# Kernel tuning notes

Hardware: AMD Instinct MI355X
Metric: run time of the kernel (lower is better)

The kernel has to match this reference:

```python
import jax, jax.numpy as jnp
import numpy as np

B, C, D, H, W = 4, 32, 64, 64, 64
RATIO = 2
K = 7  # spatial conv kernel


def setup_inputs() -> dict:
    key = jax.random.key(0)
    ks = jax.random.split(key, 7)
    x = jax.random.normal(ks[0], (B, C, D, H, W), dtype=jnp.float32)
    # ChannelAttention params (torch Linear: y = x @ W.T + b)
    fc1_w = jax.random.normal(ks[1], (2 * C * RATIO, 2 * C), dtype=jnp.float32) * 0.05
    fc1_b = jax.random.normal(ks[2], (2 * C * RATIO,), dtype=jnp.float32) * 0.05
    fc2_w = jax.random.normal(ks[3], (C, 2 * C * RATIO), dtype=jnp.float32) * 0.05
    fc2_b = jax.random.normal(ks[4], (C,), dtype=jnp.float32) * 0.05
    # SpatialAttention convs (no bias): conv1 2->4 k=7 pad 3, conv2 4->1 k=1
    conv1_w = jax.random.normal(ks[5], (2 * RATIO, 2, K, K, K), dtype=jnp.float32) * 0.05
    conv2_w = jax.random.normal(ks[6], (1, 2 * RATIO, 1, 1, 1), dtype=jnp.float32) * 0.05
    return {"x": x, "fc1_w": fc1_w, "fc1_b": fc1_b, "fc2_w": fc2_w,
            "fc2_b": fc2_b, "conv1_w": conv1_w, "conv2_w": conv2_w}


def _conv3d(x, w, padding):
    return jax.lax.conv_general_dilated(
        x, w, window_strides=(1, 1, 1), padding=padding,
        dimension_numbers=("NCDHW", "OIDHW", "NCDHW"))


def reference(x, fc1_w, fc1_b, fc2_w, fc2_b, conv1_w, conv2_w):
    # --- ChannelAttention: ca [B, C] ---
    x_avg = jnp.mean(x, axis=(2, 3, 4))  # [B, C]
    x_max = jnp.max(x, axis=(2, 3, 4))   # [B, C]
    h = jnp.concatenate([x_avg, x_max], axis=1)  # [B, 2C]
    h = jax.nn.relu(h @ fc1_w.T + fc1_b)
    ca = jax.nn.sigmoid(h @ fc2_w.T + fc2_b)     # [B, C]

    # --- SpatialAttention: sa [B, 1, D, H, W] ---
    avg_out = jnp.mean(x, axis=1, keepdims=True)
    max_out = jnp.max(x, axis=1, keepdims=True)
    s = jnp.concatenate([avg_out, max_out], axis=1)  # [B, 2, D, H, W]
    s = jax.nn.relu(_conv3d(s, conv1_w, "SAME"))     # k=7, pad=3 == SAME
    sa = jax.nn.sigmoid(_conv3d(s, conv2_w, "VALID"))  # [B, 1, D, H, W]

    # fused broadcast replacing the per-(i,j) python loop:
    # attention[b, c] = sa[b, 0] * ca[b, c]
    attention = sa * ca[:, :, None, None, None]  # [B, C, D, H, W]
    anti_attention = 1.0 - attention
    return attention, anti_attention
```

## Files before the change

### kernel.cpp

```cpp
#include <hip/hip_runtime.h>
#include <math.h>

#define Bn 4
#define Cn 32
#define Dn 64
#define Hn 64
#define Wn 64
#define HW (Hn * Wn)
#define DHW (Dn * Hn * Wn)
#define TOT (Bn * Cn * DHW)
#define NCHUNK 128
#define NWH 1372

typedef float f4 __attribute__((ext_vector_type(4)));
typedef unsigned int u32;
typedef u32 u4 __attribute__((ext_vector_type(4)));
typedef _Float16 h2 __attribute__((ext_vector_type(2)));

__device__ __forceinline__ u32 packh2(float a, float b) {
    h2 h;
    h.x = (_Float16)a;
    h.y = (_Float16)b;
    return __builtin_bit_cast(u32, h);
}
__device__ __forceinline__ h2 uash2(u32 u) { return __builtin_bit_cast(h2, u); }

__device__ __forceinline__ float dot2acc(u32 iv, u32 wv, float acc) {
#if __has_builtin(__builtin_amdgcn_fdot2)
    return __builtin_amdgcn_fdot2(uash2(iv), uash2(wv), acc, false);
#else
    const h2 a = uash2(iv), b = uash2(wv);
    return acc + (float)a.x * (float)b.x + (float)a.y * (float)b.y;
#endif
}

__global__ __launch_bounds__(256) void wpack_kernel(
    const float* __restrict__ w1, u32* __restrict__ w1h) {
    const int i = blockIdx.x * 256 + threadIdx.x;
    if (i < NWH) {
        const int oc = i / 343, r = i - oc * 343;
        w1h[i] = packh2(w1[oc * 686 + r], w1[oc * 686 + 343 + r]);
    }
}

__global__ __launch_bounds__(256) void reduce_kernel(
    const float* __restrict__ x, u32* __restrict__ s_am,
    float* __restrict__ part_sum, float* __restrict__ part_max) {
    const int b = blockIdx.x / NCHUNK;
    const int chunk = blockIdx.x % NCHUNK;
    const int base = chunk * 2048 + threadIdx.x * 4;
    const int lane = threadIdx.x & 63;
    const int wid = threadIdx.x >> 6;

    f4 ssum0 = {0.f, 0.f, 0.f, 0.f}, ssum1 = {0.f, 0.f, 0.f, 0.f};
    f4 smax0 = {-INFINITY, -INFINITY, -INFINITY, -INFINITY};
    f4 smax1 = smax0;
    float tsum[Cn], tmax[Cn];

    const float* xp = x + (size_t)b * Cn * DHW + base;
#pragma unroll
    for (int c = 0; c < Cn; ++c) {
        const f4 v0 = *reinterpret_cast<const f4*>(xp + (size_t)c * DHW);
        const f4 v1 = *reinterpret_cast<const f4*>(xp + (size_t)c * DHW + 1024);
        ssum0 += v0; ssum1 += v1;
        smax0.x = fmaxf(smax0.x, v0.x); smax0.y = fmaxf(smax0.y, v0.y);
        smax0.z = fmaxf(smax0.z, v0.z); smax0.w = fmaxf(smax0.w, v0.w);
        smax1.x = fmaxf(smax1.x, v1.x); smax1.y = fmaxf(smax1.y, v1.y);
        smax1.z = fmaxf(smax1.z, v1.z); smax1.w = fmaxf(smax1.w, v1.w);
        const float s0 = (v0.x + v0.y) + (v0.z + v0.w);
        const float s1 = (v1.x + v1.y) + (v1.z + v1.w);
        tsum[c] = s0 + s1;
        const float m0 = fmaxf(fmaxf(v0.x, v0.y), fmaxf(v0.z, v0.w));
        const float m1 = fmaxf(fmaxf(v1.x, v1.y), fmaxf(v1.z, v1.w));
        tmax[c] = fmaxf(m0, m1);
    }

    const f4 av0 = ssum0 * (1.f / Cn);
    const f4 av1 = ssum1 * (1.f / Cn);
    u4 o0 = {packh2(av0.x, smax0.x), packh2(av0.y, smax0.y),
             packh2(av0.z, smax0.z), packh2(av0.w, smax0.w)};
    u4 o1 = {packh2(av1.x, smax1.x), packh2(av1.y, smax1.y),
             packh2(av1.z, smax1.z), packh2(av1.w, smax1.w)};
    *reinterpret_cast<u4*>(s_am + (size_t)b * DHW + base) = o0;
    *reinterpret_cast<u4*>(s_am + (size_t)b * DHW + base + 1024) = o1;

    __shared__ float redS[4][Cn];
    __shared__ float redM[4][Cn];
#pragma unroll
    for (int c = 0; c < Cn; ++c) {
        float ps = tsum[c], pm = tmax[c];
#pragma unroll
        for (int off = 32; off; off >>= 1) {
            ps += __shfl_xor(ps, off);
            pm = fmaxf(pm, __shfl_xor(pm, off));
        }
        if (lane == 0) { redS[wid][c] = ps; redM[wid][c] = pm; }
    }
    __syncthreads();
    if (threadIdx.x < Cn) {
        const int c = threadIdx.x;
        float s = (redS[0][c] + redS[1][c]) + (redS[2][c] + redS[3][c]);
        float m = fmaxf(fmaxf(redM[0][c], redM[1][c]),
                        fmaxf(redM[2][c], redM[3][c]));
        part_sum[(b * Cn + c) * NCHUNK + chunk] = s;
        part_max[(b * Cn + c) * NCHUNK + chunk] = m;
    }
}

__global__ __launch_bounds__(256) void ca_kernel(
    const float* __restrict__ part_sum, const float* __restrict__ part_max,
    const float* __restrict__ fc1_w, const float* __restrict__ fc1_b,
    const float* __restrict__ fc2_w, const float* __restrict__ fc2_b,
    float* __restrict__ ca) {
    __shared__ float inpAll[Bn][64];
    __shared__ float h[128];
    const int t = threadIdx.x;
    {
        const int which = t >> 7;
        const int b = (t >> 5) & 3;
        const int c = t & 31;
        const f4* p4 = reinterpret_cast<const f4*>(
            (which ? part_max : part_sum) + (b * Cn + c) * NCHUNK);
        if (which == 0) {
            float acc = 0.f;
#pragma unroll
            for (int i = 0; i < NCHUNK / 4; ++i) {
                f4 v = p4[i];
                acc += (v.x + v.y) + (v.z + v.w);
            }
            inpAll[b][c] = acc * (1.f / DHW);
        } else {
            float m = -INFINITY;
#pragma unroll
            for (int i = 0; i < NCHUNK / 4; ++i) {
                f4 v = p4[i];
                m = fmaxf(m, fmaxf(fmaxf(v.x, v.y), fmaxf(v.z, v.w)));
            }
            inpAll[b][Cn + c] = m;
        }
    }
    __syncthreads();
#pragma unroll 1
    for (int b = 0; b < Bn; ++b) {
        if (t < 128) {
            float acc = fc1_b[t];
#pragma unroll
            for (int k = 0; k < 64; ++k) acc += fc1_w[t * 64 + k] * inpAll[b][k];
            h[t] = fmaxf(acc, 0.f);
        }
        __syncthreads();
        if (t < Cn) {
            float a2 = fc2_b[t];
#pragma unroll
            for (int k = 0; k < 128; ++k) a2 += fc2_w[t * 128 + k] * h[k];
            ca[b * Cn + t] = 1.f / (1.f + expf(-a2));
        }
        __syncthreads();
    }
}

#define TZc 4
#define TYc 4
#define LXc (Wn + 6)
#define LYc (TYc + 6)
#define LZc (TZc + 6)
#define HALO_N (LZc * LYc * LXc)

__global__ __launch_bounds__(256) void conv_kernel(
    const float* __restrict__ ca_g, const u32* __restrict__ s_am,
    const u32* __restrict__ w1h, const float* __restrict__ w2,
    float* __restrict__ out) {
    __shared__ u32 sIn[HALO_N];
    __shared__ float sv_s[TZc * TYc * Wn];
    __shared__ float ca_s[Cn];

    const int t = threadIdx.x;
    const int bid = blockIdx.x;
    const int b = bid >> 8;
    const int tile = bid & 255;
    const int tz = tile >> 4, ty = tile & 15;
    const int z0 = tz * TZc, y0 = ty * TYc;

    if (t < Cn) ca_s[t] = ca_g[b * Cn + t];

    const u32* src = s_am + (size_t)b * DHW;
    for (int i = t; i < HALO_N; i += 256) {
        const int xx = i % LXc;
        const int rem = i / LXc;
        const int yy = rem % LYc;
        const int zz = rem / LYc;
        const int gz = z0 + zz - 3, gy = y0 + yy - 3, gx = xx - 3;
        u32 v = 0u;
        if ((unsigned)gz < (unsigned)Dn && (unsigned)gy < (unsigned)Hn &&
            (unsigned)gx < (unsigned)Wn)
            v = src[(gz * Hn + gy) * Wn + gx];
        sIn[i] = v;
    }
    __syncthreads();

    const int lx = t & 63, ly = t >> 6;

    float a0[TZc] = {0.f, 0.f, 0.f, 0.f};
    float a1[TZc] = {0.f, 0.f, 0.f, 0.f};
    float a2[TZc] = {0.f, 0.f, 0.f, 0.f};
    float a3[TZc] = {0.f, 0.f, 0.f, 0.f};

#pragma unroll 1
    for (int kh = 0; kh < 7; ++kh)
#pragma unroll 1
        for (int kw = 0; kw < 7; ++kw) {
            u32 incol[LZc];
#pragma unroll
            for (int s = 0; s < LZc; ++s)
                incol[s] = sIn[(s * LYc + (ly + kh)) * LXc + (lx + kw)];
#pragma unroll
            for (int kd = 0; kd < 7; ++kd) {
                const int wi = kd * 49 + kh * 7 + kw;
                const u32 w0 = w1h[0 * 343 + wi];
                const u32 w1v = w1h[1 * 343 + wi];
                const u32 w2v = w1h[2 * 343 + wi];
                const u32 w3v = w1h[3 * 343 + wi];
#pragma unroll
                for (int o = 0; o < TZc; ++o) {
                    const u32 iv = incol[o + kd];
                    a0[o] = dot2acc(iv, w0, a0[o]);
                    a1[o] = dot2acc(iv, w1v, a1[o]);
                    a2[o] = dot2acc(iv, w2v, a2[o]);
                    a3[o] = dot2acc(iv, w3v, a3[o]);
                }
            }
        }

    const float c20 = w2[0], c21 = w2[1], c22 = w2[2], c23 = w2[3];
#pragma unroll
    for (int o = 0; o < TZc; ++o) {
        float s = fmaxf(a0[o], 0.f) * c20 + fmaxf(a1[o], 0.f) * c21 +
                  fmaxf(a2[o], 0.f) * c22 + fmaxf(a3[o], 0.f) * c23;
        sv_s[(o * TYc + ly) * Wn + lx] = 1.f / (1.f + expf(-s));
    }
    __syncthreads();

    const int wv = t >> 6, ln = t & 63;
    const f4* sv4 = reinterpret_cast<const f4*>(sv_s);
    f4* out4 = reinterpret_cast<f4*>(out);
    const size_t totq4 = TOT / 4;
#pragma unroll 1
    for (int combo = wv; combo < Cn * TZc; combo += 4) {
        const int c = combo >> 2, oz = combo & 3;
        const float cav = ca_s[c];
        const f4 v = sv4[oz * 64 + ln];
        const f4 att = v * cav;
        const f4 anti = 1.f - att;
        const size_t off = (((size_t)(b * Cn + c) * DHW) >> 2) +
                           (size_t)(z0 + oz) * (HW / 4) +
                           (size_t)y0 * (Wn / 4) + ln;
        __builtin_nontemporal_store(att, &out4[off]);
        __builtin_nontemporal_store(anti, &out4[totq4 + off]);
    }
}

extern "C" void kernel_launch(void* const* d_in, const int* in_sizes, int n_in,
                              void* d_out, int out_size, void* d_ws,
                              size_t ws_size, hipStream_t stream) {
    const float* x = (const float*)d_in[0];
    const float* fc1_w = (const float*)d_in[1];
    const float* fc1_b = (const float*)d_in[2];
    const float* fc2_w = (const float*)d_in[3];
    const float* fc2_b = (const float*)d_in[4];
    const float* conv1_w = (const float*)d_in[5];
    const float* conv2_w = (const float*)d_in[6];

    float* ws = (float*)d_ws;
    u32* s_am = (u32*)ws;
    float* part_sum = ws + (size_t)Bn * DHW;
    float* part_max = part_sum + Bn * Cn * NCHUNK;
    float* ca = part_max + Bn * Cn * NCHUNK;
    u32* w1h = (u32*)(ca + Bn * Cn);

    wpack_kernel<<<(NWH + 255) / 256, 256, 0, stream>>>(conv1_w, w1h);
    reduce_kernel<<<Bn * NCHUNK, 256, 0, stream>>>(x, s_am, part_sum,
                                                   part_max);
    ca_kernel<<<1, 256, 0, stream>>>(part_sum, part_max, fc1_w, fc1_b, fc2_w,
                                     fc2_b, ca);
    conv_kernel<<<Bn * 256, 256, 0, stream>>>(ca, s_am, w1h, conv2_w,
                                              (float*)d_out);
}
```

Measured before the change: 133.1 us.

## Fold weight packing into ca kernel, double z-tile, store outputs directly from registers

The conv1 weight fp16 packing moves into the single-block channel-attention kernel, which removes one kernel launch. The conv tile depth in z grows from 4 to 8, halving the grid to 512 blocks and increasing reuse of each loaded halo column across more outputs. The spatial-attention values now stay in registers and each thread writes scalar nontemporal stores per channel, replacing the shared-memory staging, the barrier and the float4 stores. The cost is more accumulator registers, fewer blocks for 256 CUs, and narrower scalar stores that may reduce write efficiency.

```diff
diff --git a/kernel.cpp b/kernel.cpp
--- a/kernel.cpp
+++ b/kernel.cpp
@@ -32,15 +32,6 @@
     const h2 a = uash2(iv), b = uash2(wv);
     return acc + (float)a.x * (float)b.x + (float)a.y * (float)b.y;
 #endif
-}
-
-__global__ __launch_bounds__(256) void wpack_kernel(
-    const float* __restrict__ w1, u32* __restrict__ w1h) {
-    const int i = blockIdx.x * 256 + threadIdx.x;
-    if (i < NWH) {
-        const int oc = i / 343, r = i - oc * 343;
-        w1h[i] = packh2(w1[oc * 686 + r], w1[oc * 686 + 343 + r]);
-    }
 }
 
 __global__ __launch_bounds__(256) void reduce_kernel(
@@ -108,13 +99,19 @@
 }
 
 __global__ __launch_bounds__(256) void ca_kernel(
+    const float* __restrict__ w1, u32* __restrict__ w1h,
     const float* __restrict__ part_sum, const float* __restrict__ part_max,
     const float* __restrict__ fc1_w, const float* __restrict__ fc1_b,
     const float* __restrict__ fc2_w, const float* __restrict__ fc2_b,
     float* __restrict__ ca) {
+    const int t = threadIdx.x;
+    for (int i = t; i < NWH; i += 256) {
+        const int oc = i / 343, r = i - oc * 343;
+        w1h[i] = packh2(w1[oc * 686 + r], w1[oc * 686 + 343 + r]);
+    }
+
     __shared__ float inpAll[Bn][64];
     __shared__ float h[128];
-    const int t = threadIdx.x;
     {
         const int which = t >> 7;
         const int b = (t >> 5) & 3;
@@ -159,7 +156,7 @@
     }
 }
 
-#define TZc 4
+#define TZc 8
 #define TYc 4
 #define LXc (Wn + 6)
 #define LYc (TYc + 6)
@@ -171,13 +168,12 @@
     const u32* __restrict__ w1h, const float* __restrict__ w2,
     float* __restrict__ out) {
     __shared__ u32 sIn[HALO_N];
-    __shared__ float sv_s[TZc * TYc * Wn];
     __shared__ float ca_s[Cn];
 
     const int t = threadIdx.x;
     const int bid = blockIdx.x;
-    const int b = bid >> 8;
-    const int tile = bid & 255;
+    const int b = bid >> 7;
+    const int tile = bid & 127;
     const int tz = tile >> 4, ty = tile & 15;
     const int z0 = tz * TZc, y0 = ty * TYc;
 
@@ -200,10 +196,10 @@
 
     const int lx = t & 63, ly = t >> 6;
 
-    float a0[TZc] = {0.f, 0.f, 0.f, 0.f};
-    float a1[TZc] = {0.f, 0.f, 0.f, 0.f};
-    float a2[TZc] = {0.f, 0.f, 0.f, 0.f};
-    float a3[TZc] = {0.f, 0.f, 0.f, 0.f};
+    float a0[TZc] = {0.f, 0.f, 0.f, 0.f, 0.f, 0.f, 0.f, 0.f};
+    float a1[TZc] = {0.f, 0.f, 0.f, 0.f, 0.f, 0.f, 0.f, 0.f};
+    float a2[TZc] = {0.f, 0.f, 0.f, 0.f, 0.f, 0.f, 0.f, 0.f};
+    float a3[TZc] = {0.f, 0.f, 0.f, 0.f, 0.f, 0.f, 0.f, 0.f};
 
 #pragma unroll 1
     for (int kh = 0; kh < 7; ++kh)
@@ -232,30 +228,26 @@
         }
 
     const float c20 = w2[0], c21 = w2[1], c22 = w2[2], c23 = w2[3];
+    float sv[TZc];
 #pragma unroll
     for (int o = 0; o < TZc; ++o) {
         float s = fmaxf(a0[o], 0.f) * c20 + fmaxf(a1[o], 0.f) * c21 +
                   fmaxf(a2[o], 0.f) * c22 + fmaxf(a3[o], 0.f) * c23;
-        sv_s[(o * TYc + ly) * Wn + lx] = 1.f / (1.f + expf(-s));
-    }
-    __syncthreads();
-
-    const int wv = t >> 6, ln = t & 63;
-    const f4* sv4 = reinterpret_cast<const f4*>(sv_s);
-    f4* out4 = reinterpret_cast<f4*>(out);
-    const size_t totq4 = TOT / 4;
-#pragma unroll 1
-    for (int combo = wv; combo < Cn * TZc; combo += 4) {
-        const int c = combo >> 2, oz = combo & 3;
+        sv[o] = 1.f / (1.f + expf(-s));
+    }
+
+    const size_t base = (size_t)b * Cn * DHW + (size_t)z0 * HW +
+                        (size_t)(y0 + ly) * Wn + lx;
+#pragma unroll 1
+    for (int c = 0; c < Cn; ++c) {
         const float cav = ca_s[c];
-        const f4 v = sv4[oz * 64 + ln];
-        const f4 att = v * cav;
-        const f4 anti = 1.f - att;
-        const size_t off = (((size_t)(b * Cn + c) * DHW) >> 2) +
-                           (size_t)(z0 + oz) * (HW / 4) +
-                           (size_t)y0 * (Wn / 4) + ln;
-        __builtin_nontemporal_store(att, &out4[off]);
-        __builtin_nontemporal_store(anti, &out4[totq4 + off]);
+        const size_t cb = base + (size_t)c * DHW;
+#pragma unroll
+        for (int o = 0; o < TZc; ++o) {
+            const float a = sv[o] * cav;
+            __builtin_nontemporal_store(a, out + cb + o * HW);
+            __builtin_nontemporal_store(1.f - a, out + TOT + cb + o * HW);
+        }
     }
 }
 
@@ -277,11 +269,10 @@
     float* ca = part_max + Bn * Cn * NCHUNK;
     u32* w1h = (u32*)(ca + Bn * Cn);
 
-    wpack_kernel<<<(NWH + 255) / 256, 256, 0, stream>>>(conv1_w, w1h);
     reduce_kernel<<<Bn * NCHUNK, 256, 0, stream>>>(x, s_am, part_sum,
                                                    part_max);
-    ca_kernel<<<1, 256, 0, stream>>>(part_sum, part_max, fc1_w, fc1_b, fc2_w,
-                                     fc2_b, ca);
-    conv_kernel<<<Bn * 256, 256, 0, stream>>>(ca, s_am, w1h, conv2_w,
+    ca_kernel<<<1, 256, 0, stream>>>(conv1_w, w1h, part_sum, part_max, fc1_w,
+                                     fc1_b, fc2_w, fc2_b, ca);
+    conv_kernel<<<Bn * 128, 256, 0, stream>>>(ca, s_am, w1h, conv2_w,
                                               (float*)d_out);
 }
```

Measured after the change: 150.7 us. +13.2%, slower.

## Fold weight packing into ca kernel and retile conv to two y-halves

Applied to the files above, without the earlier changes.

Removes the separate weight-packing launch by doing the fp16 packing inside the single-block channel-attention kernel. The conv kernel tile shrinks to 2 rows in y, and each block now processes two y-tiles in sequence, reloading the halo for each. Threads are remapped so each computes 2 z outputs instead of 4, which cuts accumulator registers. The store phase is adjusted to half-row columns. The cost is more halo reload traffic per output (8 rows loaded for 2 outputs instead of 10 for 4) and a serialized loop in exchange for lower register pressure and one fewer launch.

```diff
diff --git a/kernel.cpp b/kernel.cpp
--- a/kernel.cpp
+++ b/kernel.cpp
@@ -34,13 +34,9 @@
 #endif
 }
 
-__global__ __launch_bounds__(256) void wpack_kernel(
-    const float* __restrict__ w1, u32* __restrict__ w1h) {
-    const int i = blockIdx.x * 256 + threadIdx.x;
-    if (i < NWH) {
-        const int oc = i / 343, r = i - oc * 343;
-        w1h[i] = packh2(w1[oc * 686 + r], w1[oc * 686 + 343 + r]);
-    }
+__device__ __forceinline__ void lds_barrier() {
+    asm volatile("s_waitcnt lgkmcnt(0)" ::: "memory");
+    __builtin_amdgcn_s_barrier();
 }
 
 __global__ __launch_bounds__(256) void reduce_kernel(
@@ -108,13 +104,19 @@
 }
 
 __global__ __launch_bounds__(256) void ca_kernel(
+    const float* __restrict__ w1, u32* __restrict__ w1h,
     const float* __restrict__ part_sum, const float* __restrict__ part_max,
     const float* __restrict__ fc1_w, const float* __restrict__ fc1_b,
     const float* __restrict__ fc2_w, const float* __restrict__ fc2_b,
     float* __restrict__ ca) {
+    const int t = threadIdx.x;
+    for (int i = t; i < NWH; i += 256) {
+        const int oc = i / 343, r = i - oc * 343;
+        w1h[i] = packh2(w1[oc * 686 + r], w1[oc * 686 + 343 + r]);
+    }
+
     __shared__ float inpAll[Bn][64];
     __shared__ float h[128];
-    const int t = threadIdx.x;
     {
         const int which = t >> 7;
         const int b = (t >> 5) & 3;
@@ -160,7 +162,7 @@
 }
 
 #define TZc 4
-#define TYc 4
+#define TYc 2
 #define LXc (Wn + 6)
 #define LYc (TYc + 6)
 #define LZc (TZc + 6)
@@ -177,85 +179,92 @@
     const int t = threadIdx.x;
     const int bid = blockIdx.x;
     const int b = bid >> 8;
-    const int tile = bid & 255;
-    const int tz = tile >> 4, ty = tile & 15;
-    const int z0 = tz * TZc, y0 = ty * TYc;
+    const int pair = bid & 255;
+    const int tz = pair >> 4, tyh = pair & 15;
+    const int z0 = tz * TZc;
 
     if (t < Cn) ca_s[t] = ca_g[b * Cn + t];
 
     const u32* src = s_am + (size_t)b * DHW;
-    for (int i = t; i < HALO_N; i += 256) {
-        const int xx = i % LXc;
-        const int rem = i / LXc;
-        const int yy = rem % LYc;
-        const int zz = rem / LYc;
-        const int gz = z0 + zz - 3, gy = y0 + yy - 3, gx = xx - 3;
-        u32 v = 0u;
-        if ((unsigned)gz < (unsigned)Dn && (unsigned)gy < (unsigned)Hn &&
-            (unsigned)gx < (unsigned)Wn)
-            v = src[(gz * Hn + gy) * Wn + gx];
-        sIn[i] = v;
-    }
-    __syncthreads();
-
-    const int lx = t & 63, ly = t >> 6;
-
-    float a0[TZc] = {0.f, 0.f, 0.f, 0.f};
-    float a1[TZc] = {0.f, 0.f, 0.f, 0.f};
-    float a2[TZc] = {0.f, 0.f, 0.f, 0.f};
-    float a3[TZc] = {0.f, 0.f, 0.f, 0.f};
-
-#pragma unroll 1
-    for (int kh = 0; kh < 7; ++kh)
-#pragma unroll 1
-        for (int kw = 0; kw < 7; ++kw) {
-            u32 incol[LZc];
-#pragma unroll
-            for (int s = 0; s < LZc; ++s)
-                incol[s] = sIn[(s * LYc + (ly + kh)) * LXc + (lx + kw)];
-#pragma unroll
-            for (int kd = 0; kd < 7; ++kd) {
-                const int wi = kd * 49 + kh * 7 + kw;
-                const u32 w0 = w1h[0 * 343 + wi];
-                const u32 w1v = w1h[1 * 343 + wi];
-                const u32 w2v = w1h[2 * 343 + wi];
-                const u32 w3v = w1h[3 * 343 + wi];
-#pragma unroll
-                for (int o = 0; o < TZc; ++o) {
-                    const u32 iv = incol[o + kd];
-                    a0[o] = dot2acc(iv, w0, a0[o]);
-                    a1[o] = dot2acc(iv, w1v, a1[o]);
-                    a2[o] = dot2acc(iv, w2v, a2[o]);
-                    a3[o] = dot2acc(iv, w3v, a3[o]);
+    const int lx = t & 63, ly = (t >> 6) & 1, zh = t >> 7;
+    const float c20 = w2[0], c21 = w2[1], c22 = w2[2], c23 = w2[3];
+
+#pragma unroll 1
+    for (int half = 0; half < 2; ++half) {
+        const int y0 = (tyh + half * 16) * TYc;
+
+        lds_barrier();
+        for (int i = t; i < HALO_N; i += 256) {
+            const int xx = i % LXc;
+            const int rem = i / LXc;
+            const int yy = rem % LYc;
+            const int zz = rem / LYc;
+            const int gz = z0 + zz - 3, gy = y0 + yy - 3, gx = xx - 3;
+            u32 v = 0u;
+            if ((unsigned)gz < (unsigned)Dn && (unsigned)gy < (unsigned)Hn &&
+                (unsigned)gx < (unsigned)Wn)
+                v = src[(gz * Hn + gy) * Wn + gx];
+            sIn[i] = v;
+        }
+        lds_barrier();
+
+        float a0[2] = {0.f, 0.f}, a1[2] = {0.f, 0.f};
+        float a2[2] = {0.f, 0.f}, a3[2] = {0.f, 0.f};
+#pragma unroll 1
+        for (int kh = 0; kh < 7; ++kh)
+#pragma unroll 1
+            for (int kw = 0; kw < 7; ++kw) {
+                u32 incol[8];
+#pragma unroll
+                for (int s = 0; s < 8; ++s)
+                    incol[s] = sIn[((zh * 2 + s) * LYc + (ly + kh)) * LXc +
+                                   (lx + kw)];
+#pragma unroll
+                for (int kd = 0; kd < 7; ++kd) {
+                    const int wi = kd * 49 + kh * 7 + kw;
+                    const u32 w0 = w1h[0 * 343 + wi];
+                    const u32 w1v = w1h[1 * 343 + wi];
+                    const u32 w2v = w1h[2 * 343 + wi];
+                    const u32 w3v = w1h[3 * 343 + wi];
+#pragma unroll
+                    for (int o = 0; o < 2; ++o) {
+                        const u32 iv = incol[o + kd];
+                        a0[o] = dot2acc(iv, w0, a0[o]);
+                        a1[o] = dot2acc(iv, w1v, a1[o]);
+                        a2[o] = dot2acc(iv, w2v, a2[o]);
+                        a3[o] = dot2acc(iv, w3v, a3[o]);
+                    }
                 }
             }
-        }
-
-    const float c20 = w2[0], c21 = w2[1], c22 = w2[2], c23 = w2[3];
-#pragma unroll
-    for (int o = 0; o < TZc; ++o) {
-        float s = fmaxf(a0[o], 0.f) * c20 + fmaxf(a1[o], 0.f) * c21 +
-                  fmaxf(a2[o], 0.f) * c22 + fmaxf(a3[o], 0.f) * c23;
-        sv_s[(o * TYc + ly) * Wn + lx] = 1.f / (1.f + expf(-s));
-    }
-    __syncthreads();
-
-    const int wv = t >> 6, ln = t & 63;
-    const f4* sv4 = reinterpret_cast<const f4*>(sv_s);
-    f4* out4 = reinterpret_cast<f4*>(out);
-    const size_t totq4 = TOT / 4;
-#pragma unroll 1
-    for (int combo = wv; combo < Cn * TZc; combo += 4) {
-        const int c = combo >> 2, oz = combo & 3;
-        const float cav = ca_s[c];
-        const f4 v = sv4[oz * 64 + ln];
-        const f4 att = v * cav;
-        const f4 anti = 1.f - att;
-        const size_t off = (((size_t)(b * Cn + c) * DHW) >> 2) +
-                           (size_t)(z0 + oz) * (HW / 4) +
-                           (size_t)y0 * (Wn / 4) + ln;
-        __builtin_nontemporal_store(att, &out4[off]);
-        __builtin_nontemporal_store(anti, &out4[totq4 + off]);
+
+#pragma unroll
+        for (int o = 0; o < 2; ++o) {
+            const int oz = zh * 2 + o;
+            float s = fmaxf(a0[o], 0.f) * c20 + fmaxf(a1[o], 0.f) * c21 +
+                      fmaxf(a2[o], 0.f) * c22 + fmaxf(a3[o], 0.f) * c23;
+            sv_s[(oz * TYc + ly) * Wn + lx] = 1.f / (1.f + expf(-s));
+        }
+        lds_barrier();
+
+        const int wv = t >> 6, ln = t & 63;
+        const int ozh = ln >> 5, lncol = ln & 31;
+        const f4* sv4 = reinterpret_cast<const f4*>(sv_s);
+        f4* out4 = reinterpret_cast<f4*>(out);
+        const size_t totq4 = TOT / 4;
+#pragma unroll 1
+        for (int combo = wv; combo < Cn * 2; combo += 4) {
+            const int c = combo >> 1, zp = combo & 1;
+            const int oz = zp * 2 + ozh;
+            const float cav = ca_s[c];
+            const f4 v = sv4[oz * (TYc * Wn / 4) + lncol];
+            const f4 att = v * cav;
+            const f4 anti = 1.f - att;
+            const size_t off = (((size_t)(b * Cn + c) * DHW) >> 2) +
+                               (size_t)(z0 + oz) * (HW / 4) +
+                               (size_t)y0 * (Wn / 4) + lncol;
+            __builtin_nontemporal_store(att, &out4[off]);
+            __builtin_nontemporal_store(anti, &out4[totq4 + off]);
+        }
     }
 }
 
@@ -277,11 +286,10 @@
     float* ca = part_max + Bn * Cn * NCHUNK;
     u32* w1h = (u32*)(ca + Bn * Cn);
 
-    wpack_kernel<<<(NWH + 255) / 256, 256, 0, stream>>>(conv1_w, w1h);
     reduce_kernel<<<Bn * NCHUNK, 256, 0, stream>>>(x, s_am, part_sum,
                                                    part_max);
-    ca_kernel<<<1, 256, 0, stream>>>(part_sum, part_max, fc1_w, fc1_b, fc2_w,
-                                     fc2_b, ca);
+    ca_kernel<<<1, 256, 0, stream>>>(conv1_w, w1h, part_sum, part_max, fc1_w,
+                                     fc1_b, fc2_w, fc2_b, ca);
     conv_kernel<<<Bn * 256, 256, 0, stream>>>(ca, s_am, w1h, conv2_w,
                                               (float*)d_out);
 }
```

Measured after the change: 139.5 us. 4.8% more time.
